# Performance work log

Measured on AMD Instinct MI355X. Metric: run time of the kernel, lower is better.

The kernel has to match this reference:

```python
import jax, jax.numpy as jnp
import numpy as np

B, T, D = 256, 336, 128
H = 1024
N_LABEL, LABEL_CLASS = 24, 1
FORGET_BIAS = 1.0  # TF BasicLSTMCell default


def setup_inputs() -> dict:
    key = jax.random.key(0)
    ks = jax.random.split(key, 8)
    s1 = 1.0 / np.sqrt(D + H)
    s2 = 1.0 / np.sqrt(2 * H)
    sd = 1.0 / np.sqrt(H)
    return {
        "features": jax.random.normal(ks[0], (B, T, D), jnp.float32),
        "labels": jax.random.normal(ks[1], (B, N_LABEL, LABEL_CLASS), jnp.float32),
        "W1": jax.random.normal(ks[2], (D + H, 4 * H), jnp.float32) * s1,
        "b1": jnp.zeros((4 * H,), jnp.float32),
        "W2": jax.random.normal(ks[3], (2 * H, 4 * H), jnp.float32) * s2,
        "b2": jnp.zeros((4 * H,), jnp.float32),
        "Wd": jax.random.normal(ks[4], (H, N_LABEL * LABEL_CLASS), jnp.float32) * sd,
        "bd": jnp.zeros((N_LABEL * LABEL_CLASS,), jnp.float32),
    }


def _lstm_cell(c, h, x, W, b):
    # TF BasicLSTMCell: gates = [x, h] @ W + b, split into i, j, f, o
    z = jnp.concatenate([x, h], axis=-1) @ W + b
    i, j, f, o = jnp.split(z, 4, axis=-1)
    new_c = c * jax.nn.sigmoid(f + FORGET_BIAS) + jax.nn.sigmoid(i) * jnp.tanh(j)
    new_h = jnp.tanh(new_c) * jax.nn.sigmoid(o)
    return new_c, new_h


def reference(features, labels, W1, b1, W2, b2, Wd, bd):
    batch = features.shape[0]
    zeros = jnp.zeros((batch, H), features.dtype)
    init = (zeros, zeros, zeros, zeros)  # c1, h1, c2, h2

    def step(carry, x_t):
        c1, h1, c2, h2 = carry
        c1, h1 = _lstm_cell(c1, h1, x_t, W1, b1)
        c2, h2 = _lstm_cell(c2, h2, h1, W2, b2)
        return (c1, h1, c2, h2), None

    xs = jnp.swapaxes(features, 0, 1)  # [T, B, D]
    (c1, h1, c2, h2), _ = jax.lax.scan(step, init, xs)
    # dense head on last-timestep output of top layer
    pred = (h2 @ Wd + bd).reshape(batch, N_LABEL, LABEL_CLASS)
    loss = jnp.mean(jnp.square(pred - labels))
    return loss
```

## Files before the change

### kernel.cpp

```cpp
#include <hip/hip_runtime.h>

#define TT 336
#define BB 256
#define DD 128
#define HH 1024
#define TD 43008
#define BBHH 262144

#define SSU0 20480u
#define SSU1 32768u
#define LBU1 5242880u

typedef __attribute__((ext_vector_type(8))) short short8;
typedef __attribute__((ext_vector_type(8))) unsigned short ushort8;
typedef __attribute__((ext_vector_type(4))) unsigned short ushort4v;
typedef __attribute__((ext_vector_type(4))) float floatx4;

#define OFF_ZPAD 0u
#define OFF_C1   4096u
#define OFF_C2   1052672u
#define OFF_H1   2101248u
#define OFF_H2   3149824u
#define OFF_B1P  4198400u
#define OFF_B2P  4214784u
#define OFF_X    4231168u
#define OFF_BP   26251264u

static __device__ __forceinline__ unsigned short f2bf(float f) {
  unsigned int x = __float_as_uint(f);
  x += 0x7fffu + ((x >> 16) & 1u);
  return (unsigned short)(x >> 16);
}
static __device__ __forceinline__ float bf2f(unsigned short u) {
  return __uint_as_float(((unsigned int)u) << 16);
}
static __device__ __forceinline__ float sigm(float x) {
  return 1.f / (1.f + __expf(-x));
}
static __device__ __forceinline__ float tanh_fast(float x) {
  float ax = fabsf(x);
  float e = __expf(-2.f * ax);
  float t = (1.f - e) / (1.f + e);
  return x < 0.f ? -t : t;
}

#define GLOAD_LDS16(gsrc, ldst)                                              \
  __builtin_amdgcn_global_load_lds(                                          \
      (const __attribute__((address_space(1))) void*)(gsrc),                 \
      (__attribute__((address_space(3))) void*)(ldst), 16, 0, 0)

__global__ __launch_bounds__(256) void init_zero(float* out, uint4* span, long n16) {
  long i = (long)blockIdx.x * 256 + threadIdx.x;
  if (i < n16) span[i] = make_uint4(0u, 0u, 0u, 0u);
  if (i == 0) out[0] = 0.f;
}

__global__ __launch_bounds__(256) void feat2bf(const float* __restrict__ in,
                                               unsigned short* __restrict__ out, long nq) {
  long Q = (long)blockIdx.x * 256 + threadIdx.x;
  if (Q >= nq) return;
  int b = (int)(Q / 5376);
  long outQ = (Q & ~7L) | ((Q ^ (long)b) & 7);
  const floatx4* pp = (const floatx4*)(in + Q * 8);
  floatx4 a = pp[0], c = pp[1];
  ushort8 v;
  #pragma unroll
  for (int q = 0; q < 4; ++q) { v[q] = f2bf(a[q]); v[4 + q] = f2bf(c[q]); }
  *(ushort8*)(out + outQ * 8) = v;
}

__global__ __launch_bounds__(256) void bpack(const float* __restrict__ W1,
                                             const float* __restrict__ W2,
                                             unsigned short* __restrict__ out) {
  __shared__ unsigned short tile[64][72];
  int bid = blockIdx.x, t = threadIdx.x;
  int L, tk, tn;
  if (bid < 1280) { L = 0; tk = bid % 20; tn = bid / 20; }
  else            { L = 1; tk = (bid - 1280) % 32; tn = (bid - 1280) / 32; }
  const float* W = L ? W2 : W1;
  int KG = L ? 512 : 320;
  int k0 = tk * 64, n0p = tn * 64;
  int g = k0 / KG;
  int ksg0 = (k0 - g * KG) >> 5;
  int ntile = n0p >> 7, wn = (n0p >> 6) & 1;
  unsigned int SSu = L ? SSU1 : SSU0;
  unsigned int base = (L ? LBU1 : 0u) + ntile * 8u * SSu + (g * 2 + wn) * SSu;

  #pragma unroll
  for (int i = 0; i < 16; ++i) {
    int idx = i * 256 + t;
    int kk = idx >> 6, nn = idx & 63;
    int np = n0p + nn;
    int norig = ((np & 3) << 10) + (np >> 2);
    float v = 0.f;
    if (!(L == 0 && k0 + kk >= 1152)) v = W[(size_t)(k0 + kk) * 4096 + norig];
    tile[kk][nn] = f2bf(v);
  }
  __syncthreads();
  int t64 = t & 63;
  #pragma unroll
  for (int pass = 0; pass < 2; ++pass) {
    int f = (t >> 6) + pass * 4;
    int ksl = f >> 2, ni = f & 3;
    ushort8 v;
    #pragma unroll
    for (int j = 0; j < 8; ++j)
      v[j] = tile[ksl * 32 + ((t64 >> 4) << 3) + j][ni * 16 + (t64 & 15)];
    *(ushort8*)(out + base + (unsigned)((ksg0 + ksl) * 4 + ni) * 512u + t64 * 8) = v;
  }
}

__global__ __launch_bounds__(256) void bias_perm(const float* __restrict__ b1,
                                                 const float* __restrict__ b2,
                                                 float* __restrict__ b1p,
                                                 float* __restrict__ b2p) {
  int idx = blockIdx.x * 256 + threadIdx.x;
  const float* src = (idx < 4096) ? b1 : b2;
  float* dst = (idx < 4096) ? b1p : b2p;
  int n = idx & 4095;
  dst[n] = src[(n & 3) * 1024 + (n >> 2)];
}

__global__ __launch_bounds__(512, 2) void gemm_cell(
    const unsigned short* __restrict__ Xbf,
    unsigned short* __restrict__ h1bufs, unsigned short* __restrict__ h2bufs,
    const unsigned short* __restrict__ Bpack,
    const float* __restrict__ b1p, const float* __restrict__ b2p,
    float* __restrict__ c1, float* __restrict__ c2,
    const unsigned short* __restrict__ zpad,
    int p, int do1, int do2) {
  __shared__ __align__(16) unsigned short Abuf[4][2][64 * 64];
  __shared__ __align__(16) float zt0[64 * 132];
  __shared__ __align__(16) float zt1[64 * 132];

  int bid = blockIdx.x;
  int layer = bid >> 7;
  if (layer == 0 ? !do1 : !do2) return;
  int lid = bid & 127;
  int ntile = (lid & 7) | (((lid >> 5) & 3) << 3);
  int mtile = (lid >> 3) & 3;
  int m0 = mtile * 64;
  int u0 = ntile * 32;

  const unsigned short* hp1 = h1bufs + (size_t)(p & 1) * BBHH;
  const unsigned short* hp2 = h2bufs + (size_t)(p & 1) * BBHH;
  const int KG = layer ? 512 : 320;
  const int NIT = KG >> 6;

  int tid = threadIdx.x;
  int g = tid >> 7;
  int wn = (tid >> 6) & 1;
  int lane = tid & 63;
  int kgbase = g * KG;

  unsigned int SSu = layer ? SSU1 : SSU0;
  const unsigned short* bwave =
      Bpack + (layer ? LBU1 : 0u) + ntile * 8u * SSu + (unsigned)(g * 2 + wn) * SSu;

  auto stageA = [&](int buf, int it) {
    int kb = kgbase + (it << 6);
    unsigned short* dst0 = &Abuf[g][buf][0];
    #pragma unroll
    for (int c = 0; c < 4; ++c) {
      int rowbase = c * 16 + wn * 8;
      int rg = m0 + rowbase + (lane >> 3);
      int kq = lane & 7;
      const unsigned short* src;
      if (layer == 0) {
        if (kb < DD)        src = Xbf + (size_t)rg * TD + p * DD + kb + kq * 8;
        else if (kb < 1152) src = hp1 + (size_t)rg * HH + (kb - DD) + kq * 8;
        else                src = zpad + lane * 8;
      } else {
        if (kb < HH) src = hp1 + (size_t)rg * HH + kb + kq * 8;
        else         src = hp2 + (size_t)rg * HH + (kb - HH) + kq * 8;
      }
      GLOAD_LDS16(src, dst0 + rowbase * 64);
    }
  };
  auto loadB = [&](ushort8 (&dst)[2][4], int it) {
    #pragma unroll
    for (int ksl = 0; ksl < 2; ++ksl)
      #pragma unroll
      for (int ni = 0; ni < 4; ++ni)
        dst[ksl][ni] =
            *(const ushort8*)(bwave + (unsigned)((it * 2 + ksl) * 4 + ni) * 512u + lane * 8);
  };

  floatx4 acc[4][4];
  #pragma unroll
  for (int i = 0; i < 4; ++i)
    #pragma unroll
    for (int j = 0; j < 4; ++j) acc[i][j] = (floatx4){0.f, 0.f, 0.f, 0.f};

  ushort8 bc[2][4], bn[2][4];
  stageA(0, 0);
  loadB(bc, 0);

  for (int it = 0; it < NIT; ++it) {
    int buf = it & 1;
    __syncthreads();
    if (it + 1 < NIT) { stageA(buf ^ 1, it + 1); loadB(bn, it + 1); }
    const unsigned short* Ab = &Abuf[g][buf][0];
    #pragma unroll
    for (int ksl = 0; ksl < 2; ++ksl) {
      int qb = ksl * 4 + (lane >> 4);
      short8 af[4];
      #pragma unroll
      for (int mi = 0; mi < 4; ++mi) {
        int ml = mi * 16 + (lane & 15);
        af[mi] = *(const short8*)&Ab[ml * 64 + ((qb ^ (ml & 7)) << 3)];
      }
      #pragma unroll
      for (int mi = 0; mi < 4; ++mi)
        #pragma unroll
        for (int ni = 0; ni < 4; ++ni)
          acc[mi][ni] = __builtin_amdgcn_mfma_f32_16x16x32_bf16(
              af[mi], (short8)bc[ksl][ni], acc[mi][ni], 0, 0, 0);
    }
    #pragma unroll
    for (int ksl = 0; ksl < 2; ++ksl)
      #pragma unroll
      for (int ni = 0; ni < 4; ++ni) bc[ksl][ni] = bn[ksl][ni];
  }

  float* ztw = (g & 1) ? zt1 : zt0;
  if (g < 2) {
    #pragma unroll
    for (int mi = 0; mi < 4; ++mi)
      #pragma unroll
      for (int ni = 0; ni < 4; ++ni)
        #pragma unroll
        for (int rr = 0; rr < 4; ++rr) {
          int row = mi * 16 + (lane >> 4) * 4 + rr;
          int col = wn * 64 + ni * 16 + (lane & 15);
          ztw[row * 132 + col] = acc[mi][ni][rr];
        }
  }
  __syncthreads();
  if (g >= 2) {
    #pragma unroll
    for (int mi = 0; mi < 4; ++mi)
      #pragma unroll
      for (int ni = 0; ni < 4; ++ni)
        #pragma unroll
        for (int rr = 0; rr < 4; ++rr) {
          int row = mi * 16 + (lane >> 4) * 4 + rr;
          int col = wn * 64 + ni * 16 + (lane & 15);
          ztw[row * 132 + col] += acc[mi][ni][rr];
        }
  }
  __syncthreads();

  {
    unsigned short* hn = (layer ? h2bufs : h1bufs) + (size_t)((p + 1) & 1) * BBHH;
    int r = tid >> 3, ug = tid & 7;
    int rg = m0 + r;
    float* cp = (layer ? c2 : c1) + (size_t)rg * HH + u0 + ug * 4;
    const float* bp = (layer ? b2p : b1p) + (size_t)(u0 + ug * 4) * 4;
    floatx4 cold = *(const floatx4*)cp;
    floatx4 cn;
    ushort4v hv;
    #pragma unroll
    for (int k = 0; k < 4; ++k) {
      int cbase = r * 132 + (ug * 4 + k) * 4;
      floatx4 gt0 = *(const floatx4*)&zt0[cbase];
      floatx4 gt1 = *(const floatx4*)&zt1[cbase];
      floatx4 bb = *(const floatx4*)&bp[k * 4];
      float i_ = gt0[0] + gt1[0] + bb[0];
      float j_ = gt0[1] + gt1[1] + bb[1];
      float f_ = gt0[2] + gt1[2] + bb[2] + 1.f;
      float o_ = gt0[3] + gt1[3] + bb[3];
      float nc = cold[k] * sigm(f_) + sigm(i_) * tanh_fast(j_);
      cn[k] = nc;
      hv[k] = f2bf(tanh_fast(nc) * sigm(o_));
    }
    *(floatx4*)cp = cn;
    int q = (u0 >> 3) + (ug >> 1);
    *(ushort4v*)&hn[(size_t)rg * HH + (((q & ~7) | ((q ^ rg) & 7)) << 3) + (ug & 1) * 4] = hv;
  }
}

__global__ __launch_bounds__(64) void head_loss(const unsigned short* __restrict__ h2,
                                                const float* __restrict__ Wd,
                                                const float* __restrict__ bd,
                                                const float* __restrict__ labels,
                                                float* __restrict__ out) {
  int b = blockIdx.x;
  int l = threadIdx.x;
  float pacc[24];
  #pragma unroll
  for (int n = 0; n < 24; ++n) pacc[n] = 0.f;
  for (int k = l; k < HH; k += 64) {
    int ksw = (k & ~63) | ((((k >> 3) ^ b) & 7) << 3) | (k & 7);
    float hv = bf2f(h2[(size_t)b * HH + ksw]);
    const float* wr = Wd + (size_t)k * 24;
    #pragma unroll
    for (int n = 0; n < 24; ++n) pacc[n] += hv * wr[n];
  }
  #pragma unroll
  for (int n = 0; n < 24; ++n) {
    float v = pacc[n];
    for (int off = 32; off > 0; off >>= 1) v += __shfl_down(v, off);
    pacc[n] = v;
  }
  if (l == 0) {
    float s = 0.f;
    #pragma unroll
    for (int n = 0; n < 24; ++n) {
      float pred = pacc[n] + bd[n];
      float d = pred - labels[b * 24 + n];
      s += d * d;
    }
    atomicAdd(out, s * (1.0f / 6144.0f));
  }
}

extern "C" void kernel_launch(void* const* d_in, const int* in_sizes, int n_in,
                              void* d_out, int out_size, void* d_ws, size_t ws_size,
                              hipStream_t stream) {
  const float* features = (const float*)d_in[0];
  const float* labels   = (const float*)d_in[1];
  const float* W1 = (const float*)d_in[2];
  const float* b1 = (const float*)d_in[3];
  const float* W2 = (const float*)d_in[4];
  const float* b2 = (const float*)d_in[5];
  const float* Wd = (const float*)d_in[6];
  const float* bd = (const float*)d_in[7];

  char* ws = (char*)d_ws;
  unsigned short* zpad = (unsigned short*)(ws + OFF_ZPAD);
  float*          c1   = (float*)(ws + OFF_C1);
  float*          c2   = (float*)(ws + OFF_C2);
  unsigned short* h1   = (unsigned short*)(ws + OFF_H1);
  unsigned short* h2   = (unsigned short*)(ws + OFF_H2);
  float*          b1p  = (float*)(ws + OFF_B1P);
  float*          b2p  = (float*)(ws + OFF_B2P);
  unsigned short* Xbf  = (unsigned short*)(ws + OFF_X);
  unsigned short* BP   = (unsigned short*)(ws + OFF_BP);
  float* out = (float*)d_out;

  init_zero<<<1026, 256, 0, stream>>>(out, (uint4*)ws, 262400L);
  feat2bf<<<5376, 256, 0, stream>>>(features, Xbf, 1376256L);
  bpack<<<3328, 256, 0, stream>>>(W1, W2, BP);
  bias_perm<<<32, 256, 0, stream>>>(b1, b2, b1p, b2p);

  for (int p = 0; p <= TT; ++p) {
    gemm_cell<<<256, 512, 0, stream>>>(Xbf, h1, h2, BP, b1p, b2p, c1, c2, zpad,
                                       p, p < TT ? 1 : 0, p >= 1 ? 1 : 0);
  }
  head_loss<<<256, 64, 0, stream>>>(h2 + BBHH, Wd, bd, labels, out);
}
```

Measured before the change: 6.540 ms.

## Replace per-timestep kernel launches with a persistent cooperative LSTM kernel

Replaces the 337 per-step gemm_cell launches with a single cooperative persistent kernel that loops over timesteps. Blocks synchronise through per-mtile global counters using spin-waits, so each block waits only on the row group it depends on rather than on a full grid barrier. Cell state now lives in registers instead of global memory, and bias values are hoisted out of the time loop. A tiles are loaded through registers with agent-scope atomic loads instead of direct global-to-LDS loads, and the feature/h swizzle is dropped. This removes launch overhead and the c reload/store each step, but adds spin-wait latency and relies on relaxed-ordering visibility between blocks.

```diff
diff --git a/kernel.cpp b/kernel.cpp
--- a/kernel.cpp
+++ b/kernel.cpp
@@ -16,15 +16,13 @@
 typedef __attribute__((ext_vector_type(4))) unsigned short ushort4v;
 typedef __attribute__((ext_vector_type(4))) float floatx4;
 
-#define OFF_ZPAD 0u
-#define OFF_C1   4096u
-#define OFF_C2   1052672u
-#define OFF_H1   2101248u
-#define OFF_H2   3149824u
-#define OFF_B1P  4198400u
-#define OFF_B2P  4214784u
-#define OFF_X    4231168u
-#define OFF_BP   26251264u
+#define OFF_CNT 0u
+#define OFF_B1P 4096u
+#define OFF_B2P 20480u
+#define OFF_H1  65536u
+#define OFF_H2  1114112u
+#define OFF_X   2162688u
+#define OFF_BP  24182784u
 
 static __device__ __forceinline__ unsigned short f2bf(float f) {
   unsigned int x = __float_as_uint(f);
@@ -44,11 +42,6 @@
   return x < 0.f ? -t : t;
 }
 
-#define GLOAD_LDS16(gsrc, ldst)                                              \
-  __builtin_amdgcn_global_load_lds(                                          \
-      (const __attribute__((address_space(1))) void*)(gsrc),                 \
-      (__attribute__((address_space(3))) void*)(ldst), 16, 0, 0)
-
 __global__ __launch_bounds__(256) void init_zero(float* out, uint4* span, long n16) {
   long i = (long)blockIdx.x * 256 + threadIdx.x;
   if (i < n16) span[i] = make_uint4(0u, 0u, 0u, 0u);
@@ -59,14 +52,12 @@
                                                unsigned short* __restrict__ out, long nq) {
   long Q = (long)blockIdx.x * 256 + threadIdx.x;
   if (Q >= nq) return;
-  int b = (int)(Q / 5376);
-  long outQ = (Q & ~7L) | ((Q ^ (long)b) & 7);
   const floatx4* pp = (const floatx4*)(in + Q * 8);
   floatx4 a = pp[0], c = pp[1];
   ushort8 v;
   #pragma unroll
   for (int q = 0; q < 4; ++q) { v[q] = f2bf(a[q]); v[4 + q] = f2bf(c[q]); }
-  *(ushort8*)(out + outQ * 8) = v;
+  *(ushort8*)(out + Q * 8) = v;
 }
 
 __global__ __launch_bounds__(256) void bpack(const float* __restrict__ W1,
@@ -121,29 +112,24 @@
   dst[n] = src[(n & 3) * 1024 + (n >> 2)];
 }
 
-__global__ __launch_bounds__(512, 2) void gemm_cell(
+__global__ __launch_bounds__(512, 2) void lstm_persist(
     const unsigned short* __restrict__ Xbf,
     unsigned short* __restrict__ h1bufs, unsigned short* __restrict__ h2bufs,
     const unsigned short* __restrict__ Bpack,
     const float* __restrict__ b1p, const float* __restrict__ b2p,
-    float* __restrict__ c1, float* __restrict__ c2,
-    const unsigned short* __restrict__ zpad,
-    int p, int do1, int do2) {
+    unsigned int* __restrict__ cnts) {
   __shared__ __align__(16) unsigned short Abuf[4][2][64 * 64];
   __shared__ __align__(16) float zt0[64 * 132];
   __shared__ __align__(16) float zt1[64 * 132];
+  __shared__ unsigned int lds_arr;
 
   int bid = blockIdx.x;
   int layer = bid >> 7;
-  if (layer == 0 ? !do1 : !do2) return;
   int lid = bid & 127;
   int ntile = (lid & 7) | (((lid >> 5) & 3) << 3);
   int mtile = (lid >> 3) & 3;
   int m0 = mtile * 64;
   int u0 = ntile * 32;
-
-  const unsigned short* hp1 = h1bufs + (size_t)(p & 1) * BBHH;
-  const unsigned short* hp2 = h2bufs + (size_t)(p & 1) * BBHH;
   const int KG = layer ? 512 : 320;
   const int NIT = KG >> 6;
 
@@ -151,132 +137,178 @@
   int g = tid >> 7;
   int wn = (tid >> 6) & 1;
   int lane = tid & 63;
+  int gt = tid & 127;
   int kgbase = g * KG;
+  unsigned int* cnt = cnts + mtile * 64;
 
   unsigned int SSu = layer ? SSU1 : SSU0;
   const unsigned short* bwave =
       Bpack + (layer ? LBU1 : 0u) + ntile * 8u * SSu + (unsigned)(g * 2 + wn) * SSu;
 
-  auto stageA = [&](int buf, int it) {
-    int kb = kgbase + (it << 6);
-    unsigned short* dst0 = &Abuf[g][buf][0];
-    #pragma unroll
-    for (int c = 0; c < 4; ++c) {
-      int rowbase = c * 16 + wn * 8;
-      int rg = m0 + rowbase + (lane >> 3);
-      int kq = lane & 7;
-      const unsigned short* src;
-      if (layer == 0) {
-        if (kb < DD)        src = Xbf + (size_t)rg * TD + p * DD + kb + kq * 8;
-        else if (kb < 1152) src = hp1 + (size_t)rg * HH + (kb - DD) + kq * 8;
-        else                src = zpad + lane * 8;
-      } else {
-        if (kb < HH) src = hp1 + (size_t)rg * HH + kb + kq * 8;
-        else         src = hp2 + (size_t)rg * HH + (kb - HH) + kq * 8;
-      }
-      GLOAD_LDS16(src, dst0 + rowbase * 64);
+  if (tid == 0) lds_arr = 0u;
+
+  int rr_ = tid >> 3, ugc = tid & 7;
+  int rgc = m0 + rr_;
+  floatx4 creg = (floatx4){0.f, 0.f, 0.f, 0.f};
+  const float* bpb = (layer ? b2p : b1p) + (size_t)(u0 + ugc * 4) * 4;
+  floatx4 bpr[4];
+  #pragma unroll
+  for (int k = 0; k < 4; ++k) bpr[k] = *(const floatx4*)&bpb[k * 4];
+  __syncthreads();
+
+  ushort8 bc[2][4], bn[2][4], areg[4];
+
+  for (int p = 0; p <= TT; ++p) {
+    bool active = layer == 0 ? (p < TT) : (p >= 1);
+    const unsigned short* hp1 = h1bufs + (size_t)(p & 1) * BBHH;
+    const unsigned short* hp2 = h2bufs + (size_t)(p & 1) * BBHH;
+
+    auto loadB = [&](ushort8 (&dst)[2][4], int it) {
+      #pragma unroll
+      for (int ksl = 0; ksl < 2; ++ksl)
+        #pragma unroll
+        for (int ni = 0; ni < 4; ++ni)
+          dst[ksl][ni] = *(const ushort8*)(bwave +
+              (unsigned)((it * 2 + ksl) * 4 + ni) * 512u + lane * 8);
+    };
+    auto issueA = [&](int it) {
+      int kb = kgbase + (it << 6);
+      #pragma unroll
+      for (int c = 0; c < 4; ++c) {
+        int rg = m0 + c * 16 + (gt >> 3);
+        int kq = gt & 7;
+        if (layer == 0 && kb < DD) {
+          areg[c] = *(const ushort8*)(Xbf + (size_t)rg * TD + p * DD + kb + kq * 8);
+        } else if (layer == 0 && kb >= 1152) {
+          areg[c] = (ushort8){0, 0, 0, 0, 0, 0, 0, 0};
+        } else {
+          const unsigned short* src;
+          if (layer == 0)      src = hp1 + (size_t)rg * HH + (kb - DD) + kq * 8;
+          else if (kb < HH)    src = hp1 + (size_t)rg * HH + kb + kq * 8;
+          else                 src = hp2 + (size_t)rg * HH + (kb - HH) + kq * 8;
+          union { unsigned long long u[2]; ushort8 v; } uu;
+          uu.u[0] = __hip_atomic_load((const unsigned long long*)src,
+                                      __ATOMIC_RELAXED, __HIP_MEMORY_SCOPE_AGENT);
+          uu.u[1] = __hip_atomic_load((const unsigned long long*)(src + 4),
+                                      __ATOMIC_RELAXED, __HIP_MEMORY_SCOPE_AGENT);
+          areg[c] = uu.v;
+        }
+      }
+    };
+    auto commitA = [&](int buf) {
+      unsigned short* dst = &Abuf[g][buf][0];
+      #pragma unroll
+      for (int c = 0; c < 4; ++c) {
+        int row = c * 16 + (gt >> 3);
+        int kq = gt & 7;
+        *(ushort8*)&dst[row * 64 + ((kq ^ (row & 7)) << 3)] = areg[c];
+      }
+    };
+
+    if (active) loadB(bc, 0);
+
+    if (p > 0) {
+      if (lane == 0) {
+        unsigned int tgt = 64u * (unsigned)p;
+        while (__hip_atomic_load(cnt, __ATOMIC_RELAXED, __HIP_MEMORY_SCOPE_AGENT) < tgt)
+          __builtin_amdgcn_s_sleep(2);
+      }
     }
-  };
-  auto loadB = [&](ushort8 (&dst)[2][4], int it) {
-    #pragma unroll
-    for (int ksl = 0; ksl < 2; ++ksl)
-      #pragma unroll
-      for (int ni = 0; ni < 4; ++ni)
-        dst[ksl][ni] =
-            *(const ushort8*)(bwave + (unsigned)((it * 2 + ksl) * 4 + ni) * 512u + lane * 8);
-  };
-
-  floatx4 acc[4][4];
-  #pragma unroll
-  for (int i = 0; i < 4; ++i)
-    #pragma unroll
-    for (int j = 0; j < 4; ++j) acc[i][j] = (floatx4){0.f, 0.f, 0.f, 0.f};
-
-  ushort8 bc[2][4], bn[2][4];
-  stageA(0, 0);
-  loadB(bc, 0);
-
-  for (int it = 0; it < NIT; ++it) {
-    int buf = it & 1;
-    __syncthreads();
-    if (it + 1 < NIT) { stageA(buf ^ 1, it + 1); loadB(bn, it + 1); }
-    const unsigned short* Ab = &Abuf[g][buf][0];
-    #pragma unroll
-    for (int ksl = 0; ksl < 2; ++ksl) {
-      int qb = ksl * 4 + (lane >> 4);
-      short8 af[4];
-      #pragma unroll
-      for (int mi = 0; mi < 4; ++mi) {
-        int ml = mi * 16 + (lane & 15);
-        af[mi] = *(const short8*)&Ab[ml * 64 + ((qb ^ (ml & 7)) << 3)];
-      }
-      #pragma unroll
-      for (int mi = 0; mi < 4; ++mi)
-        #pragma unroll
-        for (int ni = 0; ni < 4; ++ni)
-          acc[mi][ni] = __builtin_amdgcn_mfma_f32_16x16x32_bf16(
-              af[mi], (short8)bc[ksl][ni], acc[mi][ni], 0, 0, 0);
+
+    if (active) {
+      floatx4 acc[4][4];
+      #pragma unroll
+      for (int i = 0; i < 4; ++i)
+        #pragma unroll
+        for (int j = 0; j < 4; ++j) acc[i][j] = (floatx4){0.f, 0.f, 0.f, 0.f};
+
+      issueA(0);
+      commitA(0);
+      for (int it = 0; it < NIT; ++it) {
+        int buf = it & 1;
+        __syncthreads();
+        if (it + 1 < NIT) { issueA(it + 1); loadB(bn, it + 1); }
+        const unsigned short* Ab = &Abuf[g][buf][0];
+        #pragma unroll
+        for (int ksl = 0; ksl < 2; ++ksl) {
+          int qb = ksl * 4 + (lane >> 4);
+          short8 af[4];
+          #pragma unroll
+          for (int mi = 0; mi < 4; ++mi) {
+            int ml = mi * 16 + (lane & 15);
+            af[mi] = *(const short8*)&Ab[ml * 64 + ((qb ^ (ml & 7)) << 3)];
+          }
+          #pragma unroll
+          for (int mi = 0; mi < 4; ++mi)
+            #pragma unroll
+            for (int ni = 0; ni < 4; ++ni)
+              acc[mi][ni] = __builtin_amdgcn_mfma_f32_16x16x32_bf16(
+                  af[mi], (short8)bc[ksl][ni], acc[mi][ni], 0, 0, 0);
+        }
+        if (it + 1 < NIT) {
+          commitA(buf ^ 1);
+          #pragma unroll
+          for (int ksl = 0; ksl < 2; ++ksl)
+            #pragma unroll
+            for (int ni = 0; ni < 4; ++ni) bc[ksl][ni] = bn[ksl][ni];
+        }
+      }
+      __syncthreads();
+
+      float* ztw = (g & 1) ? zt1 : zt0;
+      if (g < 2) {
+        #pragma unroll
+        for (int mi = 0; mi < 4; ++mi)
+          #pragma unroll
+          for (int ni = 0; ni < 4; ++ni)
+            #pragma unroll
+            for (int rr = 0; rr < 4; ++rr) {
+              int row = mi * 16 + (lane >> 4) * 4 + rr;
+              int col = wn * 64 + ni * 16 + (lane & 15);
+              ztw[row * 132 + col] = acc[mi][ni][rr];
+            }
+      }
+      __syncthreads();
+      if (g >= 2) {
+        #pragma unroll
+        for (int mi = 0; mi < 4; ++mi)
+          #pragma unroll
+          for (int ni = 0; ni < 4; ++ni)
+            #pragma unroll
+            for (int rr = 0; rr < 4; ++rr) {
+              int row = mi * 16 + (lane >> 4) * 4 + rr;
+              int col = wn * 64 + ni * 16 + (lane & 15);
+              ztw[row * 132 + col] += acc[mi][ni][rr];
+            }
+      }
+      __syncthreads();
+
+      unsigned short* hn = (layer ? h2bufs : h1bufs) + (size_t)((p + 1) & 1) * BBHH;
+      ushort4v hv;
+      #pragma unroll
+      for (int k = 0; k < 4; ++k) {
+        int cbase = rr_ * 132 + (ugc * 4 + k) * 4;
+        floatx4 gt0 = *(const floatx4*)&zt0[cbase];
+        floatx4 gt1 = *(const floatx4*)&zt1[cbase];
+        float i_ = gt0[0] + gt1[0] + bpr[k][0];
+        float j_ = gt0[1] + gt1[1] + bpr[k][1];
+        float f_ = gt0[2] + gt1[2] + bpr[k][2] + 1.f;
+        float o_ = gt0[3] + gt1[3] + bpr[k][3];
+        float nc = creg[k] * sigm(f_) + sigm(i_) * tanh_fast(j_);
+        creg[k] = nc;
+        hv[k] = f2bf(tanh_fast(nc) * sigm(o_));
+      }
+      union { ushort4v v; unsigned long long u; } hu;
+      hu.v = hv;
+      __hip_atomic_store((unsigned long long*)&hn[(size_t)rgc * HH + u0 + ugc * 4],
+                         hu.u, __ATOMIC_RELAXED, __HIP_MEMORY_SCOPE_AGENT);
     }
-    #pragma unroll
-    for (int ksl = 0; ksl < 2; ++ksl)
-      #pragma unroll
-      for (int ni = 0; ni < 4; ++ni) bc[ksl][ni] = bn[ksl][ni];
-  }
-
-  float* ztw = (g & 1) ? zt1 : zt0;
-  if (g < 2) {
-    #pragma unroll
-    for (int mi = 0; mi < 4; ++mi)
-      #pragma unroll
-      for (int ni = 0; ni < 4; ++ni)
-        #pragma unroll
-        for (int rr = 0; rr < 4; ++rr) {
-          int row = mi * 16 + (lane >> 4) * 4 + rr;
-          int col = wn * 64 + ni * 16 + (lane & 15);
-          ztw[row * 132 + col] = acc[mi][ni][rr];
-        }
-  }
-  __syncthreads();
-  if (g >= 2) {
-    #pragma unroll
-    for (int mi = 0; mi < 4; ++mi)
-      #pragma unroll
-      for (int ni = 0; ni < 4; ++ni)
-        #pragma unroll
-        for (int rr = 0; rr < 4; ++rr) {
-          int row = mi * 16 + (lane >> 4) * 4 + rr;
-          int col = wn * 64 + ni * 16 + (lane & 15);
-          ztw[row * 132 + col] += acc[mi][ni][rr];
-        }
-  }
-  __syncthreads();
-
-  {
-    unsigned short* hn = (layer ? h2bufs : h1bufs) + (size_t)((p + 1) & 1) * BBHH;
-    int r = tid >> 3, ug = tid & 7;
-    int rg = m0 + r;
-    float* cp = (layer ? c2 : c1) + (size_t)rg * HH + u0 + ug * 4;
-    const float* bp = (layer ? b2p : b1p) + (size_t)(u0 + ug * 4) * 4;
-    floatx4 cold = *(const floatx4*)cp;
-    floatx4 cn;
-    ushort4v hv;
-    #pragma unroll
-    for (int k = 0; k < 4; ++k) {
-      int cbase = r * 132 + (ug * 4 + k) * 4;
-      floatx4 gt0 = *(const floatx4*)&zt0[cbase];
-      floatx4 gt1 = *(const floatx4*)&zt1[cbase];
-      floatx4 bb = *(const floatx4*)&bp[k * 4];
-      float i_ = gt0[0] + gt1[0] + bb[0];
-      float j_ = gt0[1] + gt1[1] + bb[1];
-      float f_ = gt0[2] + gt1[2] + bb[2] + 1.f;
-      float o_ = gt0[3] + gt1[3] + bb[3];
-      float nc = cold[k] * sigm(f_) + sigm(i_) * tanh_fast(j_);
-      cn[k] = nc;
-      hv[k] = f2bf(tanh_fast(nc) * sigm(o_));
+
+    asm volatile("s_waitcnt vmcnt(0)" ::: "memory");
+    if (lane == 0) {
+      unsigned int old = atomicAdd(&lds_arr, 1u);
+      if (old == 8u * (unsigned)p + 7u) atomicAdd(cnt, 1u);
     }
-    *(floatx4*)cp = cn;
-    int q = (u0 >> 3) + (ug >> 1);
-    *(ushort4v*)&hn[(size_t)rg * HH + (((q & ~7) | ((q ^ rg) & 7)) << 3) + (ug & 1) * 4] = hv;
   }
 }
 
@@ -291,8 +323,7 @@
   #pragma unroll
   for (int n = 0; n < 24; ++n) pacc[n] = 0.f;
   for (int k = l; k < HH; k += 64) {
-    int ksw = (k & ~63) | ((((k >> 3) ^ b) & 7) << 3) | (k & 7);
-    float hv = bf2f(h2[(size_t)b * HH + ksw]);
+    float hv = bf2f(h2[(size_t)b * HH + k]);
     const float* wr = Wd + (size_t)k * 24;
     #pragma unroll
     for (int n = 0; n < 24; ++n) pacc[n] += hv * wr[n];
@@ -328,25 +359,23 @@
   const float* bd = (const float*)d_in[7];
 
   char* ws = (char*)d_ws;
-  unsigned short* zpad = (unsigned short*)(ws + OFF_ZPAD);
-  float*          c1   = (float*)(ws + OFF_C1);
-  float*          c2   = (float*)(ws + OFF_C2);
+  unsigned int*   cnts = (unsigned int*)(ws + OFF_CNT);
+  float*          b1p  = (float*)(ws + OFF_B1P);
+  float*          b2p  = (float*)(ws + OFF_B2P);
   unsigned short* h1   = (unsigned short*)(ws + OFF_H1);
   unsigned short* h2   = (unsigned short*)(ws + OFF_H2);
-  float*          b1p  = (float*)(ws + OFF_B1P);
-  float*          b2p  = (float*)(ws + OFF_B2P);
   unsigned short* Xbf  = (unsigned short*)(ws + OFF_X);
   unsigned short* BP   = (unsigned short*)(ws + OFF_BP);
   float* out = (float*)d_out;
 
-  init_zero<<<1026, 256, 0, stream>>>(out, (uint4*)ws, 262400L);
+  init_zero<<<528, 256, 0, stream>>>(out, (uint4*)ws, 135168L);
   feat2bf<<<5376, 256, 0, stream>>>(features, Xbf, 1376256L);
   bpack<<<3328, 256, 0, stream>>>(W1, W2, BP);
   bias_perm<<<32, 256, 0, stream>>>(b1, b2, b1p, b2p);
 
-  for (int p = 0; p <= TT; ++p) {
-    gemm_cell<<<256, 512, 0, stream>>>(Xbf, h1, h2, BP, b1p, b2p, c1, c2, zpad,
-                                       p, p < TT ? 1 : 0, p >= 1 ? 1 : 0);
-  }
+  void* args[] = {&Xbf, &h1, &h2, &BP, &b1p, &b2p, &cnts};
+  hipLaunchCooperativeKernel((const void*)lstm_persist, dim3(256), dim3(512),
+                             args, 0, stream);
+
   head_loss<<<256, 64, 0, stream>>>(h2 + BBHH, Wd, bd, labels, out);
 }
```

New measurement: 8.165 ms. +24.9%, slower.
